# Kernel tuning notes

Measured on AMD Instinct MI355X. Metric: run time of the kernel, lower is better.

## Reference

```python
import jax, jax.numpy as jnp
import numpy as np

N, E = 100000, 1600000
IN, HID, HEADS, OUT = 128, 16, 4, 64
SLOPE = 0.2  # leaky_relu negative_slope default


def setup_inputs() -> dict:
    key = jax.random.key(0)
    ks = jax.random.split(key, 12)
    s = 0.1  # xavier-ish scale
    return {
        "x": jax.random.normal(ks[0], (N, IN), jnp.float32),
        "edge_index": jax.random.randint(ks[1], (2, E), 0, N, jnp.int32),
        "W1": jax.random.normal(ks[2], (IN, HEADS * HID), jnp.float32) * s,
        "att_l1": jax.random.normal(ks[3], (1, HEADS, HID), jnp.float32) * s,
        "att_r1": jax.random.normal(ks[4], (1, HEADS, HID), jnp.float32) * s,
        "res_W1": jax.random.normal(ks[5], (IN, HEADS * HID), jnp.float32) * s,
        "b1": jnp.zeros((HEADS * HID,), jnp.float32),
        "W2": jax.random.normal(ks[6], (HEADS * HID, OUT), jnp.float32) * s,
        "att_l2": jax.random.normal(ks[7], (1, 1, OUT), jnp.float32) * s,
        "att_r2": jax.random.normal(ks[8], (1, 1, OUT), jnp.float32) * s,
        "b2": jnp.zeros((OUT,), jnp.float32),
    }


def agdn_conv(x, W, att_l, att_r, bias, res_W, src, dst):
    # x: [n, in]; W: [in, H*C]; att_*: [1, H, C]
    n = x.shape[0]
    H, C = att_l.shape[1], att_l.shape[2]
    x_lin = (x @ W).reshape(n, H, C)
    # residual: res_fc if present, else identity on x_lin (residual=True path)
    x_res = (x @ res_W) if res_W is not None else x_lin.reshape(n, H * C)
    al = jnp.sum(x_lin * att_l, axis=-1)  # [n, H]
    ar = jnp.sum(x_lin * att_r, axis=-1)  # [n, H]
    logits = jax.nn.leaky_relu(al[src] + ar[dst], SLOPE)  # [E, H]
    # segment softmax over incoming edges of each dst node
    m = jax.ops.segment_max(logits, dst, num_segments=n)
    e = jnp.exp(logits - m[dst])
    ssum = jax.ops.segment_sum(e, dst, num_segments=n)
    alpha = e / (ssum[dst] + 1e-16)  # [E, H]
    msg = x_lin[src] * alpha[:, :, None]  # [E, H, C]
    out = jax.ops.segment_sum(msg, dst, num_segments=n).reshape(n, H * C)
    return out + x_res + bias


def reference(x, edge_index, W1, att_l1, att_r1, res_W1, b1, W2, att_l2, att_r2, b2):
    src, dst = edge_index[0], edge_index[1]
    h = agdn_conv(x, W1, att_l1, att_r1, b1, res_W1, src, dst)
    h = jax.nn.elu(h)
    # last layer: heads=1, in==heads*out so res_fc is None (residual = x_lin)
    return agdn_conv(h, W2, att_l2, att_r2, b2, None, src, dst)
```

## Files before the change

kernel.cpp:

```cpp
#include <hip/hip_runtime.h>
#include <hip/hip_bf16.h>
#include <hip/hip_fp16.h>
#include <math.h>

#define NN 100000
#define EE 1600000
#define IN_DIM 128
#define HID 16
#define HEADS 4
#define D1 64
#define OUT_DIM 64
#define SLOPE 0.2f

#define NB 391
#define BCAP 5120
#define BINA_CHUNK 4096
#define BINA_BLOCKS ((EE + BINA_CHUNK - 1) / BINA_CHUNK)
#define NODE_BLOCKS ((NN + 63) / 64)
#define AGG_BLOCKS (NN / 32)

#define W1COLS 144
#define LDB1 272
#define LDB2 144

typedef __attribute__((ext_vector_type(8))) short bf16x8;
typedef __attribute__((ext_vector_type(4))) float f32x4;

__device__ __forceinline__ float leaky(float v) { return v > 0.f ? v : SLOPE * v; }
__device__ __forceinline__ unsigned short f2bf(float f) {
    __hip_bfloat16 h = __float2bfloat16(f);
    return *(unsigned short*)&h;
}
__device__ __forceinline__ __half2 u2h2(unsigned u) {
    union { unsigned u; __half2 h; } c; c.u = u; return c.h;
}
__device__ __forceinline__ bf16x8 pack8(float4 a, float4 b) {
    bf16x8 r;
    r[0] = (short)f2bf(a.x); r[1] = (short)f2bf(a.y);
    r[2] = (short)f2bf(a.z); r[3] = (short)f2bf(a.w);
    r[4] = (short)f2bf(b.x); r[5] = (short)f2bf(b.y);
    r[6] = (short)f2bf(b.z); r[7] = (short)f2bf(b.w);
    return r;
}

__global__ void prep_kernel(int* __restrict__ bucket_cursor,
                            const float* __restrict__ W1,
                            const float* __restrict__ resW,
                            const float* __restrict__ W2,
                            const float* __restrict__ attl1,
                            const float* __restrict__ attr1,
                            const float* __restrict__ attl2,
                            const float* __restrict__ attr2,
                            unsigned short* __restrict__ Wtb,
                            unsigned short* __restrict__ W2tb,
                            float* __restrict__ vl, float* __restrict__ vr) {
    int t = threadIdx.x;
    if (blockIdx.x == 0) {
        if (t < NB) bucket_cursor[t] = t * BCAP;
    } else if (blockIdx.x == 1) {
        for (int idx = t; idx < W1COLS * 128; idx += 512) {
            int col = idx >> 7, k = idx & 127;
            float w = 0.f;
            if (col < 64) {
                w = W1[k * 64 + col];
            } else if (col < 128) {
                w = resW[k * 64 + (col - 64)];
            } else if (col < 132) {
                int hh = col - 128;
                for (int c = 0; c < HID; c++)
                    w += W1[k * 64 + hh * HID + c] * attl1[hh * HID + c];
            } else if (col < 136) {
                int hh = col - 132;
                for (int c = 0; c < HID; c++)
                    w += W1[k * 64 + hh * HID + c] * attr1[hh * HID + c];
            }
            Wtb[idx] = f2bf(w);
        }
    } else {
        for (int idx = t; idx < 64 * 64; idx += 512) {
            int col = idx >> 6, k = idx & 63;
            W2tb[idx] = f2bf(W2[k * 64 + col]);
        }
        if (t < D1) {
            float a = 0.f, b = 0.f;
            for (int o = 0; o < OUT_DIM; o++) {
                float w = W2[t * OUT_DIM + o];
                a += w * attl2[o];
                b += w * attr2[o];
            }
            vl[t] = a; vr[t] = b;
        }
    }
}

__device__ __forceinline__ void binA_body(char* smem, int bid,
        const int* __restrict__ src, const int* __restrict__ dst,
        int* __restrict__ bucket_cursor, unsigned* __restrict__ binned) {
    int* lhist = (int*)smem;
    int* lcur  = lhist + 512;
    int* gbase = lcur + 512;
    int t = threadIdx.x;
    lhist[t] = 0; lhist[t + 256] = 0;
    lcur[t] = 0;  lcur[t + 256] = 0;
    __syncthreads();
    int e0 = bid * BINA_CHUNK;
    unsigned pk[16];
    unsigned short bk[16];
#pragma unroll
    for (int i = 0; i < 16; i++) {
        int e = e0 + t + i * 256;
        if (e < EE) {
            int d = dst[e], s = src[e];
            int b = d >> 8;
            pk[i] = ((unsigned)(d & 255) << 24) | (unsigned)s;
            bk[i] = (unsigned short)b;
            atomicAdd(&lhist[b], 1);
        } else bk[i] = 0xFFFFu;
    }
    __syncthreads();
    int c1 = lhist[t], c2 = lhist[t + 256];
    if (c1) gbase[t] = atomicAdd(&bucket_cursor[t], c1);
    if (c2) gbase[t + 256] = atomicAdd(&bucket_cursor[t + 256], c2);
    __syncthreads();
#pragma unroll
    for (int i = 0; i < 16; i++) {
        if (bk[i] != 0xFFFFu) {
            int b = bk[i];
            int pos = atomicAdd(&lcur[b], 1);
            int idx = gbase[b] + pos;
            if (idx < (b + 1) * BCAP) binned[idx] = pk[i];
        }
    }
}

__device__ __forceinline__ void node1_body(char* smemB, int bid,
        const float* __restrict__ x, const unsigned short* __restrict__ Wtb,
        const float* __restrict__ b1, __half* __restrict__ xlin1h,
        __half* __restrict__ acc1h, float* __restrict__ al1,
        float* __restrict__ ar1) {
    int t = threadIdx.x;
    int base = bid * 64;
    int wave = t >> 6, lane = t & 63;
    int quad = lane >> 4, li = lane & 15;
    int node = base + wave * 16 + li;

    uint4 breg[9];
#pragma unroll
    for (int s = 0; s < 9; s++) {
        int seg = s * 256 + t;
        breg[s] = *(const uint4*)(Wtb + (seg >> 4) * 128 + (seg & 15) * 8);
    }
    float4 xreg[8];
#pragma unroll
    for (int i = 0; i < 8; i++) xreg[i] = make_float4(0.f, 0.f, 0.f, 0.f);
    if (node < NN) {
        const float* xp = x + (size_t)node * IN_DIM + quad * 8;
#pragma unroll
        for (int kc = 0; kc < 4; kc++) {
            xreg[kc * 2]     = *(const float4*)(xp + kc * 32);
            xreg[kc * 2 + 1] = *(const float4*)(xp + kc * 32 + 4);
        }
    }
#pragma unroll
    for (int s = 0; s < 9; s++) {
        int seg = s * 256 + t;
        *(uint4*)(smemB + (seg >> 4) * LDB1 + (seg & 15) * 16) = breg[s];
    }
    __syncthreads();

    f32x4 accs[9];
#pragma unroll
    for (int nt = 0; nt < 9; nt++) accs[nt] = (f32x4){0.f, 0.f, 0.f, 0.f};
#pragma unroll
    for (int kc = 0; kc < 4; kc++) {
        bf16x8 afrag = pack8(xreg[kc * 2], xreg[kc * 2 + 1]);
        const char* brow = smemB + kc * 64 + quad * 16;
#pragma unroll
        for (int nt = 0; nt < 9; nt++) {
            bf16x8 bfrag = *(const bf16x8*)(brow + (nt * 16 + li) * LDB1);
            accs[nt] = __builtin_amdgcn_mfma_f32_16x16x32_bf16(afrag, bfrag, accs[nt], 0, 0, 0);
        }
    }

    __syncthreads();
    __half* sx = (__half*)smemB;
    __half* sa = sx + 64 * 64;
#pragma unroll
    for (int nt = 0; nt < 4; nt++) {
#pragma unroll
        for (int j = 0; j < 4; j++) {
            int rl = wave * 16 + quad * 4 + j;
            sx[rl * 64 + nt * 16 + li] = __float2half(accs[nt][j]);
        }
    }
#pragma unroll
    for (int nt = 4; nt < 8; nt++) {
        int col = (nt - 4) * 16 + li;
        float bv = b1[col];
#pragma unroll
        for (int j = 0; j < 4; j++) {
            int rl = wave * 16 + quad * 4 + j;
            sa[rl * 64 + col] = __float2half(accs[nt][j] + bv);
        }
    }
    __syncthreads();
    for (int i = t; i < 512; i += 256) {
        int row = i >> 3, seg = i & 7;
        int nd = base + row;
        if (nd < NN) {
            *(uint4*)(xlin1h + (size_t)nd * D1 + seg * 8) =
                *(const uint4*)(sx + row * 64 + seg * 8);
            *(uint4*)(acc1h + (size_t)nd * D1 + seg * 8) =
                *(const uint4*)(sa + row * 64 + seg * 8);
        }
    }
    int m0 = base + wave * 16;
#pragma unroll
    for (int j = 0; j < 4; j++) {
        int nd = m0 + quad * 4 + j;
        if (nd < NN) {
            if (li < 4) al1[nd * HEADS + li] = accs[8][j];
            else if (li < 8) ar1[nd * HEADS + (li - 4)] = accs[8][j];
        }
    }
}

__global__ __launch_bounds__(256, 4) void fusedA_kernel(
        const int* __restrict__ src, const int* __restrict__ dst,
        int* __restrict__ bucket_cursor, unsigned* __restrict__ binned,
        const float* __restrict__ x, const unsigned short* __restrict__ Wtb,
        const float* __restrict__ b1, __half* __restrict__ xlin1h,
        __half* __restrict__ acc1h, float* __restrict__ al1,
        float* __restrict__ ar1) {
    __shared__ __align__(16) char smem[W1COLS * LDB1];
    if (blockIdx.x < BINA_BLOCKS)
        binA_body(smem, blockIdx.x, src, dst, bucket_cursor, binned);
    else
        node1_body(smem, blockIdx.x - BINA_BLOCKS, x, Wtb, b1, xlin1h, acc1h, al1, ar1);
}

__global__ __launch_bounds__(256) void binB_kernel(const unsigned* __restrict__ binned,
                                                   const int* __restrict__ bucket_cursor,
                                                   int* __restrict__ row_ptr,
                                                   int* __restrict__ counts,
                                                   int* __restrict__ sorted_src) {
    __shared__ int lcount[256], lrow[256], lcur[256];
    __shared__ int wtot[4];
    int b = blockIdx.x, t = threadIdx.x;
    int start = b * BCAP;
    int cnt = bucket_cursor[b] - start;
    if (cnt > BCAP) cnt = BCAP;
    lcount[t] = 0;
    __syncthreads();
    for (int i = t; i < cnt; i += 256) {
        atomicAdd(&lcount[binned[start + i] >> 24], 1);
    }
    __syncthreads();
    int v = lcount[t];
    int lane = t & 63, wv = t >> 6;
    int inc = v;
#pragma unroll
    for (int off = 1; off < 64; off <<= 1) {
        int n = __shfl_up(inc, off, 64);
        if (lane >= off) inc += n;
    }
    if (lane == 63) wtot[wv] = inc;
    __syncthreads();
    int wbase = 0;
#pragma unroll
    for (int i = 0; i < 4; i++) if (i < wv) wbase += wtot[i];
    int ex = wbase + inc - v;
    lrow[t] = ex;
    lcur[t] = 0;
    int node = (b << 8) + t;
    if (node < NN) {
        row_ptr[node] = start + ex;
        counts[node] = v;
    }
    __syncthreads();
    for (int i = t; i < cnt; i += 256) {
        unsigned p = binned[start + i];
        int low = p >> 24;
        int pos = atomicAdd(&lcur[low], 1);
        sorted_src[start + lrow[low] + pos] = (int)(p & 0xFFFFFFu);
    }
}

__global__ __launch_bounds__(256) void agg1_kernel(
        const int* __restrict__ sorted_src, const int* __restrict__ row_ptr,
        const int* __restrict__ counts,
        const float* __restrict__ al1, const float* __restrict__ ar1,
        const __half* __restrict__ xlin1h, const __half* __restrict__ acc1h,
        __half* __restrict__ hh,
        const float* __restrict__ vl, const float* __restrict__ vr,
        float* __restrict__ al2, float* __restrict__ ar2) {
    __shared__ __half s_alpha[4][8][65][4];
    int w = threadIdx.x >> 6, lane = threadIdx.x & 63;
    int g = lane >> 3, li = lane & 7;
    int d = blockIdx.x * 32 + w * 8 + g;
    int rs = row_ptr[d];
    int deg = counts[d];
    const float4 arv = *(const float4*)(ar1 + d * 4);
    int h = li >> 1;

    int maxdeg = deg;
    maxdeg = max(maxdeg, __shfl_xor(maxdeg, 8, 64));
    maxdeg = max(maxdeg, __shfl_xor(maxdeg, 16, 64));
    maxdeg = max(maxdeg, __shfl_xor(maxdeg, 32, 64));
    bool big = maxdeg > 64;

    float s0 = 0.f, s1 = 0.f, s2 = 0.f, s3 = 0.f;
    if (!big) {
#pragma unroll
        for (int it = 0; it < 8; it++) {
            int e = li + it * 8;
            if (e < deg) {
                int s = sorted_src[rs + e];
                const float4 alv = *(const float4*)(al1 + s * 4);
                float e0 = __expf(leaky(alv.x + arv.x));
                float e1 = __expf(leaky(alv.y + arv.y));
                float e2 = __expf(leaky(alv.z + arv.z));
                float e3 = __expf(leaky(alv.w + arv.w));
                s0 += e0; s1 += e1; s2 += e2; s3 += e3;
                __half2 h01 = __floats2half2_rn(e0, e1);
                __half2 h23 = __floats2half2_rn(e2, e3);
                *(uint2*)&s_alpha[w][g][e][0] =
                    make_uint2(*(unsigned*)&h01, *(unsigned*)&h23);
            }
        }
    } else {
        for (int e = li; e < deg; e += 8) {
            int s = sorted_src[rs + e];
            const float4 alv = *(const float4*)(al1 + s * 4);
            s0 += __expf(leaky(alv.x + arv.x));
            s1 += __expf(leaky(alv.y + arv.y));
            s2 += __expf(leaky(alv.z + arv.z));
            s3 += __expf(leaky(alv.w + arv.w));
        }
    }
#pragma unroll
    for (int off = 1; off < 8; off <<= 1) {
        s0 += __shfl_xor(s0, off, 64);
        s1 += __shfl_xor(s1, off, 64);
        s2 += __shfl_xor(s2, off, 64);
        s3 += __shfl_xor(s3, off, 64);
    }
    float inv0 = 0.f, inv1 = 0.f, inv2 = 0.f, inv3 = 0.f;
    if (deg > 0) {
        inv0 = 1.f / (s0 + 1e-16f); inv1 = 1.f / (s1 + 1e-16f);
        inv2 = 1.f / (s2 + 1e-16f); inv3 = 1.f / (s3 + 1e-16f);
    }
    float invh = (h == 0) ? inv0 : (h == 1) ? inv1 : (h == 2) ? inv2 : inv3;
    __half2 invh2 = __floats2half2_rn(invh, invh);

    __half2 a01 = __floats2half2_rn(0.f, 0.f);
    __half2 a23 = a01, a45 = a01, a67 = a01;
    float fb0=0.f, fb1=0.f, fb2=0.f, fb3=0.f, fb4=0.f, fb5=0.f, fb6=0.f, fb7=0.f;
    if (!big) {
        for (int i0 = 0; i0 < maxdeg; i0 += 8) {
            int myi = i0 + li;
            int mys = (myi < deg) ? sorted_src[rs + myi] : 0;
            int ss[8]; __half ah[8]; uint4 uu[8];
#pragma unroll
            for (int j = 0; j < 8; j++) {
                ss[j] = __shfl(mys, (g << 3) + j, 64);
                int i = i0 + j;
                ah[j] = (i < deg) ? s_alpha[w][g][i][h] : __float2half(0.f);
            }
#pragma unroll
            for (int j = 0; j < 8; j++) {
                int i = i0 + j;
                uu[j] = make_uint4(0u, 0u, 0u, 0u);
                if (i < deg) uu[j] = *(const uint4*)(xlin1h + (size_t)ss[j] * D1 + li * 8);
            }
#pragma unroll
            for (int j = 0; j < 8; j++) {
                __half2 a2 = __hmul2(__half2half2(ah[j]), invh2);
                a01 = __hfma2(a2, u2h2(uu[j].x), a01);
                a23 = __hfma2(a2, u2h2(uu[j].y), a23);
                a45 = __hfma2(a2, u2h2(uu[j].z), a45);
                a67 = __hfma2(a2, u2h2(uu[j].w), a67);
            }
        }
    } else {
        float arh = (h == 0) ? arv.x : (h == 1) ? arv.y : (h == 2) ? arv.z : arv.w;
        for (int i = 0; i < deg; i++) {
            int s = sorted_src[rs + i];
            const float4 alv = *(const float4*)(al1 + s * 4);
            float lv = (h == 0) ? alv.x : (h == 1) ? alv.y : (h == 2) ? alv.z : alv.w;
            float a = __expf(leaky(lv + arh)) * invh;
            uint4 u = *(const uint4*)(xlin1h + (size_t)s * D1 + li * 8);
            float2 x01 = __half22float2(u2h2(u.x));
            float2 x23 = __half22float2(u2h2(u.y));
            float2 x45 = __half22float2(u2h2(u.z));
            float2 x67 = __half22float2(u2h2(u.w));
            fb0 += a * x01.x; fb1 += a * x01.y; fb2 += a * x23.x; fb3 += a * x23.y;
            fb4 += a * x45.x; fb5 += a * x45.y; fb6 += a * x67.x; fb7 += a * x67.y;
        }
    }
    float c0, c1, c2, c3, c4, c5, c6, c7;
    { float2 tv;
      tv = __half22float2(a01); c0 = tv.x + fb0; c1 = tv.y + fb1;
      tv = __half22float2(a23); c2 = tv.x + fb2; c3 = tv.y + fb3;
      tv = __half22float2(a45); c4 = tv.x + fb4; c5 = tv.y + fb5;
      tv = __half22float2(a67); c6 = tv.x + fb6; c7 = tv.y + fb7; }
    uint4 rres = *(const uint4*)(acc1h + (size_t)d * D1 + li * 8);
    { float2 tv;
      tv = __half22float2(u2h2(rres.x)); c0 += tv.x; c1 += tv.y;
      tv = __half22float2(u2h2(rres.y)); c2 += tv.x; c3 += tv.y;
      tv = __half22float2(u2h2(rres.z)); c4 += tv.x; c5 += tv.y;
      tv = __half22float2(u2h2(rres.w)); c6 += tv.x; c7 += tv.y; }
    c0 = c0 > 0.f ? c0 : (__expf(c0) - 1.f);
    c1 = c1 > 0.f ? c1 : (__expf(c1) - 1.f);
    c2 = c2 > 0.f ? c2 : (__expf(c2) - 1.f);
    c3 = c3 > 0.f ? c3 : (__expf(c3) - 1.f);
    c4 = c4 > 0.f ? c4 : (__expf(c4) - 1.f);
    c5 = c5 > 0.f ? c5 : (__expf(c5) - 1.f);
    c6 = c6 > 0.f ? c6 : (__expf(c6) - 1.f);
    c7 = c7 > 0.f ? c7 : (__expf(c7) - 1.f);
    __half2 o01 = __floats2half2_rn(c0, c1);
    __half2 o23 = __floats2half2_rn(c2, c3);
    __half2 o45 = __floats2half2_rn(c4, c5);
    __half2 o67 = __floats2half2_rn(c6, c7);
    uint4 hv = make_uint4(*(unsigned*)&o01, *(unsigned*)&o23,
                          *(unsigned*)&o45, *(unsigned*)&o67);
    *(uint4*)(hh + (size_t)d * D1 + li * 8) = hv;
    const float4 vla = *(const float4*)(vl + li * 8);
    const float4 vlb = *(const float4*)(vl + li * 8 + 4);
    const float4 vra = *(const float4*)(vr + li * 8);
    const float4 vrb = *(const float4*)(vr + li * 8 + 4);
    float pl = c0 * vla.x + c1 * vla.y + c2 * vla.z + c3 * vla.w
             + c4 * vlb.x + c5 * vlb.y + c6 * vlb.z + c7 * vlb.w;
    float pr = c0 * vra.x + c1 * vra.y + c2 * vra.z + c3 * vra.w
             + c4 * vrb.x + c5 * vrb.y + c6 * vrb.z + c7 * vrb.w;
#pragma unroll
    for (int off = 1; off < 8; off <<= 1) {
        pl += __shfl_xor(pl, off, 64);
        pr += __shfl_xor(pr, off, 64);
    }
    if (li == 0) { al2[d] = pl; ar2[d] = pr; }
}

__global__ __launch_bounds__(256) void agg2_kernel(
        const int* __restrict__ sorted_src, const int* __restrict__ row_ptr,
        const int* __restrict__ counts,
        const float* __restrict__ al2, const float* __restrict__ ar2,
        const __half* __restrict__ hh,
        unsigned short* __restrict__ hsum) {
    __shared__ __half s_alpha[4][8][65];
    __shared__ int    s_src[4][8][65];
    int w = threadIdx.x >> 6, lane = threadIdx.x & 63;
    int g = lane >> 3, li = lane & 7;
    int d = blockIdx.x * 32 + w * 8 + g;
    int rs = row_ptr[d];
    int deg = counts[d];
    float ard = ar2[d];

    int maxdeg = deg;
    maxdeg = max(maxdeg, __shfl_xor(maxdeg, 8, 64));
    maxdeg = max(maxdeg, __shfl_xor(maxdeg, 16, 64));
    maxdeg = max(maxdeg, __shfl_xor(maxdeg, 32, 64));
    bool big = maxdeg > 64;

    float ssum = 0.f;
    if (!big) {
#pragma unroll
        for (int it = 0; it < 8; it++) {
            int e = li + it * 8;
            if (e < deg) {
                int s = sorted_src[rs + e];
                float ex = __expf(leaky(al2[s] + ard));
                ssum += ex;
                s_alpha[w][g][e] = __float2half(ex);
                s_src[w][g][e] = s;
            }
        }
    } else {
        for (int e = li; e < deg; e += 8) {
            int s = sorted_src[rs + e];
            ssum += __expf(leaky(al2[s] + ard));
        }
    }
#pragma unroll
    for (int off = 1; off < 8; off <<= 1) ssum += __shfl_xor(ssum, off, 64);
    float inv = (deg > 0) ? 1.f / (ssum + 1e-16f) : 0.f;
    __half2 inv2h = __floats2half2_rn(inv, inv);

    __half2 a01 = __floats2half2_rn(0.f, 0.f);
    __half2 a23 = a01, a45 = a01, a67 = a01;
    float fb0=0.f, fb1=0.f, fb2=0.f, fb3=0.f, fb4=0.f, fb5=0.f, fb6=0.f, fb7=0.f;
    if (!big) {
        for (int i0 = 0; i0 < maxdeg; i0 += 8) {
            int ss[8]; __half ah[8]; uint4 uu[8];
#pragma unroll
            for (int j = 0; j < 8; j++) {
                int i = i0 + j;
                bool v = i < deg;
                ss[j] = v ? s_src[w][g][i] : 0;
                ah[j] = v ? s_alpha[w][g][i] : __float2half(0.f);
            }
#pragma unroll
            for (int j = 0; j < 8; j++) {
                int i = i0 + j;
                uu[j] = make_uint4(0u, 0u, 0u, 0u);
                if (i < deg) uu[j] = *(const uint4*)(hh + (size_t)ss[j] * D1 + li * 8);
            }
#pragma unroll
            for (int j = 0; j < 8; j++) {
                __half2 a2 = __hmul2(__half2half2(ah[j]), inv2h);
                a01 = __hfma2(a2, u2h2(uu[j].x), a01);
                a23 = __hfma2(a2, u2h2(uu[j].y), a23);
                a45 = __hfma2(a2, u2h2(uu[j].z), a45);
                a67 = __hfma2(a2, u2h2(uu[j].w), a67);
            }
        }
    } else {
        for (int i = 0; i < deg; i++) {
            int s = sorted_src[rs + i];
            float a = __expf(leaky(al2[s] + ard)) * inv;
            uint4 u = *(const uint4*)(hh + (size_t)s * D1 + li * 8);
            float2 x01 = __half22float2(u2h2(u.x));
            float2 x23 = __half22float2(u2h2(u.y));
            float2 x45 = __half22float2(u2h2(u.z));
            float2 x67 = __half22float2(u2h2(u.w));
            fb0 += a * x01.x; fb1 += a * x01.y; fb2 += a * x23.x; fb3 += a * x23.y;
            fb4 += a * x45.x; fb5 += a * x45.y; fb6 += a * x67.x; fb7 += a * x67.y;
        }
    }
    float c0, c1, c2, c3, c4, c5, c6, c7;
    { float2 tv;
      tv = __half22float2(a01); c0 = tv.x + fb0; c1 = tv.y + fb1;
      tv = __half22float2(a23); c2 = tv.x + fb2; c3 = tv.y + fb3;
      tv = __half22float2(a45); c4 = tv.x + fb4; c5 = tv.y + fb5;
      tv = __half22float2(a67); c6 = tv.x + fb6; c7 = tv.y + fb7; }
    uint4 own = *(const uint4*)(hh + (size_t)d * D1 + li * 8);
    { float2 tv;
      tv = __half22float2(u2h2(own.x)); c0 += tv.x; c1 += tv.y;
      tv = __half22float2(u2h2(own.y)); c2 += tv.x; c3 += tv.y;
      tv = __half22float2(u2h2(own.z)); c4 += tv.x; c5 += tv.y;
      tv = __half22float2(u2h2(own.w)); c6 += tv.x; c7 += tv.y; }
    union { unsigned short us[8]; uint4 u4; } hw;
    hw.us[0] = f2bf(c0); hw.us[1] = f2bf(c1); hw.us[2] = f2bf(c2); hw.us[3] = f2bf(c3);
    hw.us[4] = f2bf(c4); hw.us[5] = f2bf(c5); hw.us[6] = f2bf(c6); hw.us[7] = f2bf(c7);
    *(uint4*)(hsum + (size_t)d * D1 + li * 8) = hw.u4;
}

__global__ __launch_bounds__(256) void node3_kernel(
        const unsigned short* __restrict__ hsum,
        const unsigned short* __restrict__ W2tb,
        const float* __restrict__ b2,
        float* __restrict__ out) {
    __shared__ char smemB[64 * LDB2];
    int t = threadIdx.x;
    int base = blockIdx.x * 64;
    int wave = t >> 6, lane = t & 63;
    int quad = lane >> 4, li = lane & 15;
    int node = base + wave * 16 + li;

    uint4 breg[2];
#pragma unroll
    for (int s = 0; s < 2; s++) {
        int seg = s * 256 + t;
        breg[s] = *(const uint4*)(W2tb + (seg >> 3) * 64 + (seg & 7) * 8);
    }
    bf16x8 afr[2];
#pragma unroll
    for (int kc = 0; kc < 2; kc++)
#pragma unroll
        for (int i = 0; i < 8; i++) afr[kc][i] = 0;
    if (node < NN) {
        afr[0] = *(const bf16x8*)(hsum + (size_t)node * D1 + quad * 8);
        afr[1] = *(const bf16x8*)(hsum + (size_t)node * D1 + 32 + quad * 8);
    }
#pragma unroll
    for (int s = 0; s < 2; s++) {
        int seg = s * 256 + t;
        *(uint4*)(smemB + (seg >> 3) * LDB2 + (seg & 7) * 16) = breg[s];
    }
    __syncthreads();

    f32x4 accs[4];
#pragma unroll
    for (int nt = 0; nt < 4; nt++) accs[nt] = (f32x4){0.f, 0.f, 0.f, 0.f};
#pragma unroll
    for (int kc = 0; kc < 2; kc++) {
        const char* brow = smemB + kc * 64 + quad * 16;
#pragma unroll
        for (int nt = 0; nt < 4; nt++) {
            bf16x8 bfrag = *(const bf16x8*)(brow + (nt * 16 + li) * LDB2);
            accs[nt] = __builtin_amdgcn_mfma_f32_16x16x32_bf16(afr[kc], bfrag, accs[nt], 0, 0, 0);
        }
    }

    int m0 = base + wave * 16;
#pragma unroll
    for (int nt = 0; nt < 4; nt++) {
        int col = nt * 16 + li;
        float bv = b2[col];
#pragma unroll
        for (int j = 0; j < 4; j++) {
            int nd = m0 + quad * 4 + j;
            if (nd < NN) out[(size_t)nd * OUT_DIM + col] = accs[nt][j] + bv;
        }
    }
}

extern "C" void kernel_launch(void* const* d_in, const int* in_sizes, int n_in,
                              void* d_out, int out_size, void* d_ws, size_t ws_size,
                              hipStream_t stream) {
    const float* x     = (const float*)d_in[0];
    const int*   eidx  = (const int*)d_in[1];
    const float* W1    = (const float*)d_in[2];
    const float* attl1 = (const float*)d_in[3];
    const float* attr1 = (const float*)d_in[4];
    const float* resW1 = (const float*)d_in[5];
    const float* b1    = (const float*)d_in[6];
    const float* W2    = (const float*)d_in[7];
    const float* attl2 = (const float*)d_in[8];
    const float* attr2 = (const float*)d_in[9];
    const float* b2    = (const float*)d_in[10];

    const int* src = eidx;
    const int* dst = eidx + EE;

    __half* xlin1h = (__half*)d_ws;
    __half* acc1h  = xlin1h + (size_t)NN * D1;
    __half* hh     = acc1h + (size_t)NN * D1;
    unsigned short* hsum = (unsigned short*)(hh + (size_t)NN * D1);
    float* al1   = (float*)(hsum + (size_t)NN * D1);
    float* ar1   = al1 + (size_t)NN * HEADS;
    float* al2   = ar1 + (size_t)NN * HEADS;
    float* ar2   = al2 + NN;
    float* vl    = ar2 + NN;
    float* vr    = vl + D1;
    unsigned short* Wtb  = (unsigned short*)(vr + D1);
    unsigned short* W2tb = Wtb + W1COLS * 128;
    int* counts        = (int*)(W2tb + 64 * 64);
    int* row_ptr       = counts + NN;
    int* bucket_cursor = row_ptr + NN;
    int* sorted_src    = bucket_cursor + 512;
    unsigned* binned = (unsigned*)d_out;

    float* out = (float*)d_out;

    prep_kernel<<<3, 512, 0, stream>>>(bucket_cursor, W1, resW1, W2,
                                       attl1, attr1, attl2, attr2,
                                       Wtb, W2tb, vl, vr);
    fusedA_kernel<<<BINA_BLOCKS + NODE_BLOCKS, 256, 0, stream>>>(
        src, dst, bucket_cursor, binned,
        x, Wtb, b1, xlin1h, acc1h, al1, ar1);
    binB_kernel<<<NB, 256, 0, stream>>>(binned, bucket_cursor,
                                        row_ptr, counts, sorted_src);

    agg1_kernel<<<AGG_BLOCKS, 256, 0, stream>>>(sorted_src, row_ptr, counts,
                                                al1, ar1, xlin1h, acc1h, hh,
                                                vl, vr, al2, ar2);

    agg2_kernel<<<AGG_BLOCKS, 256, 0, stream>>>(sorted_src, row_ptr, counts,
                                                al2, ar2, hh, hsum);
    node3_kernel<<<NODE_BLOCKS, 256, 0, stream>>>(hsum, W2tb, b2, out);
}
```

Baseline: 243.2 us.

## Sort nodes by degree within block for wave balance; pad shared staging rows

Inside each 32-node block of both aggregation kernels, nodes are ranked by in-degree and assigned so each wave's 8 nodes have similar degrees. The first softmax loop now runs only to the group's maximum degree instead of a fixed 8 iterations. This is meant to cut divergence and wasted iterations in waves that mix low- and high-degree nodes. Separately, the GEMM epilogue's shared staging rows are padded from 64 to 72 halves to reduce LDS bank conflicts. The cost is an extra shuffle-based ranking pass, a block barrier, and gathered rather than contiguous node indices.

After: 244.2 us. About the same (+0.4%).

```diff
diff --git a/kernel.cpp b/kernel.cpp
--- a/kernel.cpp
+++ b/kernel.cpp
@@ -22,6 +22,7 @@
 #define W1COLS 144
 #define LDB1 272
 #define LDB2 144
+#define SEPI 72
 
 typedef __attribute__((ext_vector_type(8))) short bf16x8;
 typedef __attribute__((ext_vector_type(4))) float f32x4;
@@ -184,13 +185,13 @@
 
     __syncthreads();
     __half* sx = (__half*)smemB;
-    __half* sa = sx + 64 * 64;
+    __half* sa = sx + 64 * SEPI;
 #pragma unroll
     for (int nt = 0; nt < 4; nt++) {
 #pragma unroll
         for (int j = 0; j < 4; j++) {
             int rl = wave * 16 + quad * 4 + j;
-            sx[rl * 64 + nt * 16 + li] = __float2half(accs[nt][j]);
+            sx[rl * SEPI + nt * 16 + li] = __float2half(accs[nt][j]);
         }
     }
 #pragma unroll
@@ -200,7 +201,7 @@
 #pragma unroll
         for (int j = 0; j < 4; j++) {
             int rl = wave * 16 + quad * 4 + j;
-            sa[rl * 64 + col] = __float2half(accs[nt][j] + bv);
+            sa[rl * SEPI + col] = __float2half(accs[nt][j] + bv);
         }
     }
     __syncthreads();
@@ -209,9 +210,9 @@
         int nd = base + row;
         if (nd < NN) {
             *(uint4*)(xlin1h + (size_t)nd * D1 + seg * 8) =
-                *(const uint4*)(sx + row * 64 + seg * 8);
+                *(const uint4*)(sx + row * SEPI + seg * 8);
             *(uint4*)(acc1h + (size_t)nd * D1 + seg * 8) =
-                *(const uint4*)(sa + row * 64 + seg * 8);
+                *(const uint4*)(sa + row * SEPI + seg * 8);
         }
     }
     int m0 = base + wave * 16;
@@ -295,9 +296,21 @@
         const float* __restrict__ vl, const float* __restrict__ vr,
         float* __restrict__ al2, float* __restrict__ ar2) {
     __shared__ __half s_alpha[4][8][65][4];
-    int w = threadIdx.x >> 6, lane = threadIdx.x & 63;
+    __shared__ int s_ord[32];
+    int t = threadIdx.x;
+    int w = t >> 6, lane = t & 63;
     int g = lane >> 3, li = lane & 7;
-    int d = blockIdx.x * 32 + w * 8 + g;
+    if (t < 32) {
+        int myd = counts[blockIdx.x * 32 + t];
+        int rank = 0;
+        for (int j = 0; j < 32; j++) {
+            int dj = __shfl(myd, j, 64);
+            rank += (dj > myd) || (dj == myd && j < t);
+        }
+        s_ord[rank] = t;
+    }
+    __syncthreads();
+    int d = blockIdx.x * 32 + s_ord[w * 8 + g];
     int rs = row_ptr[d];
     int deg = counts[d];
     const float4 arv = *(const float4*)(ar1 + d * 4);
@@ -311,9 +324,7 @@
 
     float s0 = 0.f, s1 = 0.f, s2 = 0.f, s3 = 0.f;
     if (!big) {
-#pragma unroll
-        for (int it = 0; it < 8; it++) {
-            int e = li + it * 8;
+        for (int e = li; e < maxdeg; e += 8) {
             if (e < deg) {
                 int s = sorted_src[rs + e];
                 const float4 alv = *(const float4*)(al1 + s * 4);
@@ -449,9 +460,21 @@
         unsigned short* __restrict__ hsum) {
     __shared__ __half s_alpha[4][8][65];
     __shared__ int    s_src[4][8][65];
-    int w = threadIdx.x >> 6, lane = threadIdx.x & 63;
+    __shared__ int s_ord[32];
+    int t = threadIdx.x;
+    int w = t >> 6, lane = t & 63;
     int g = lane >> 3, li = lane & 7;
-    int d = blockIdx.x * 32 + w * 8 + g;
+    if (t < 32) {
+        int myd = counts[blockIdx.x * 32 + t];
+        int rank = 0;
+        for (int j = 0; j < 32; j++) {
+            int dj = __shfl(myd, j, 64);
+            rank += (dj > myd) || (dj == myd && j < t);
+        }
+        s_ord[rank] = t;
+    }
+    __syncthreads();
+    int d = blockIdx.x * 32 + s_ord[w * 8 + g];
     int rs = row_ptr[d];
     int deg = counts[d];
     float ard = ar2[d];
@@ -464,9 +487,7 @@
 
     float ssum = 0.f;
     if (!big) {
-#pragma unroll
-        for (int it = 0; it < 8; it++) {
-            int e = li + it * 8;
+        for (int e = li; e < maxdeg; e += 8) {
             if (e < deg) {
                 int s = sorted_src[rs + e];
                 float ex = __expf(leaky(al2[s] + ard));
```

## Halve W1 staging LDS footprint, raise occupancy, bound edge loops by max degree

Applied to the files above, without the earlier changes.

Node-transform GEMM now stages the transposed W1 in two K-halves through a smaller LDS buffer, which removes the 9 register-held uint4 prefetches. Launch bounds rise from 4 to 7 blocks per SM, and the output staging rows get padded (stride 72) to reduce LDS bank conflicts. The small-degree softmax loops in both aggregation kernels now stop at the group's max degree instead of always running 8 unrolled iterations. The cost is an extra pair of barriers per half, serialised global-to-LDS loads, and loss of full unrolling in the edge loops.

Result: slower. 290.0 us (+19.2%).

```diff
diff --git a/kernel.cpp b/kernel.cpp
--- a/kernel.cpp
+++ b/kernel.cpp
@@ -20,8 +20,9 @@
 #define AGG_BLOCKS (NN / 32)
 
 #define W1COLS 144
-#define LDB1 272
+#define LDBH 144
 #define LDB2 144
+#define SEPI 72
 
 typedef __attribute__((ext_vector_type(8))) short bf16x8;
 typedef __attribute__((ext_vector_type(4))) float f32x4;
@@ -144,12 +145,6 @@
     int quad = lane >> 4, li = lane & 15;
     int node = base + wave * 16 + li;
 
-    uint4 breg[9];
-#pragma unroll
-    for (int s = 0; s < 9; s++) {
-        int seg = s * 256 + t;
-        breg[s] = *(const uint4*)(Wtb + (seg >> 4) * 128 + (seg & 15) * 8);
-    }
     float4 xreg[8];
 #pragma unroll
     for (int i = 0; i < 8; i++) xreg[i] = make_float4(0.f, 0.f, 0.f, 0.f);
@@ -161,36 +156,41 @@
             xreg[kc * 2 + 1] = *(const float4*)(xp + kc * 32 + 4);
         }
     }
-#pragma unroll
-    for (int s = 0; s < 9; s++) {
-        int seg = s * 256 + t;
-        *(uint4*)(smemB + (seg >> 4) * LDB1 + (seg & 15) * 16) = breg[s];
-    }
-    __syncthreads();
 
     f32x4 accs[9];
 #pragma unroll
     for (int nt = 0; nt < 9; nt++) accs[nt] = (f32x4){0.f, 0.f, 0.f, 0.f};
-#pragma unroll
-    for (int kc = 0; kc < 4; kc++) {
-        bf16x8 afrag = pack8(xreg[kc * 2], xreg[kc * 2 + 1]);
-        const char* brow = smemB + kc * 64 + quad * 16;
-#pragma unroll
-        for (int nt = 0; nt < 9; nt++) {
-            bf16x8 bfrag = *(const bf16x8*)(brow + (nt * 16 + li) * LDB1);
-            accs[nt] = __builtin_amdgcn_mfma_f32_16x16x32_bf16(afrag, bfrag, accs[nt], 0, 0, 0);
-        }
-    }
-
-    __syncthreads();
+
+#pragma unroll
+    for (int half = 0; half < 2; half++) {
+        for (int i = t; i < W1COLS * 8; i += 256) {
+            int row = i >> 3, seg = i & 7;
+            *(uint4*)(smemB + row * LDBH + seg * 16) =
+                *(const uint4*)(Wtb + row * 128 + half * 64 + seg * 8);
+        }
+        __syncthreads();
+#pragma unroll
+        for (int kcl = 0; kcl < 2; kcl++) {
+            int kc = half * 2 + kcl;
+            bf16x8 afrag = pack8(xreg[kc * 2], xreg[kc * 2 + 1]);
+            const char* brow = smemB + kcl * 64 + quad * 16;
+#pragma unroll
+            for (int nt = 0; nt < 9; nt++) {
+                bf16x8 bfrag = *(const bf16x8*)(brow + (nt * 16 + li) * LDBH);
+                accs[nt] = __builtin_amdgcn_mfma_f32_16x16x32_bf16(afrag, bfrag, accs[nt], 0, 0, 0);
+            }
+        }
+        __syncthreads();
+    }
+
     __half* sx = (__half*)smemB;
-    __half* sa = sx + 64 * 64;
+    __half* sa = sx + 64 * SEPI;
 #pragma unroll
     for (int nt = 0; nt < 4; nt++) {
 #pragma unroll
         for (int j = 0; j < 4; j++) {
             int rl = wave * 16 + quad * 4 + j;
-            sx[rl * 64 + nt * 16 + li] = __float2half(accs[nt][j]);
+            sx[rl * SEPI + nt * 16 + li] = __float2half(accs[nt][j]);
         }
     }
 #pragma unroll
@@ -200,7 +200,7 @@
 #pragma unroll
         for (int j = 0; j < 4; j++) {
             int rl = wave * 16 + quad * 4 + j;
-            sa[rl * 64 + col] = __float2half(accs[nt][j] + bv);
+            sa[rl * SEPI + col] = __float2half(accs[nt][j] + bv);
         }
     }
     __syncthreads();
@@ -209,9 +209,9 @@
         int nd = base + row;
         if (nd < NN) {
             *(uint4*)(xlin1h + (size_t)nd * D1 + seg * 8) =
-                *(const uint4*)(sx + row * 64 + seg * 8);
+                *(const uint4*)(sx + row * SEPI + seg * 8);
             *(uint4*)(acc1h + (size_t)nd * D1 + seg * 8) =
-                *(const uint4*)(sa + row * 64 + seg * 8);
+                *(const uint4*)(sa + row * SEPI + seg * 8);
         }
     }
     int m0 = base + wave * 16;
@@ -225,14 +225,14 @@
     }
 }
 
-__global__ __launch_bounds__(256, 4) void fusedA_kernel(
+__global__ __launch_bounds__(256, 7) void fusedA_kernel(
         const int* __restrict__ src, const int* __restrict__ dst,
         int* __restrict__ bucket_cursor, unsigned* __restrict__ binned,
         const float* __restrict__ x, const unsigned short* __restrict__ Wtb,
         const float* __restrict__ b1, __half* __restrict__ xlin1h,
         __half* __restrict__ acc1h, float* __restrict__ al1,
         float* __restrict__ ar1) {
-    __shared__ __align__(16) char smem[W1COLS * LDB1];
+    __shared__ __align__(16) char smem[W1COLS * LDBH];
     if (blockIdx.x < BINA_BLOCKS)
         binA_body(smem, blockIdx.x, src, dst, bucket_cursor, binned);
     else
@@ -311,9 +311,7 @@
 
     float s0 = 0.f, s1 = 0.f, s2 = 0.f, s3 = 0.f;
     if (!big) {
-#pragma unroll
-        for (int it = 0; it < 8; it++) {
-            int e = li + it * 8;
+        for (int e = li; e < maxdeg; e += 8) {
             if (e < deg) {
                 int s = sorted_src[rs + e];
                 const float4 alv = *(const float4*)(al1 + s * 4);
@@ -464,9 +462,7 @@
 
     float ssum = 0.f;
     if (!big) {
-#pragma unroll
-        for (int it = 0; it < 8; it++) {
-            int e = li + it * 8;
+        for (int e = li; e < maxdeg; e += 8) {
             if (e < deg) {
                 int s = sorted_src[rs + e];
                 float ex = __expf(leaky(al2[s] + ard));
```
